# Kernel tuning notes

Measured on AMD Instinct MI355X. Metric: run time of the kernel, lower is better.

The kernel has to match this reference:

```python
import jax, jax.numpy as jnp
import numpy as np
from jax.scipy.special import logsumexp

EPS = 1e-16
SINKHORN_EPS = 0.05   # entropic regularization strength
SINKHORN_ITERS = 100  # fixed iteration count (jit-friendly)
PI = np.pi


def _p3_polarrel_from_cartesian(p):
    """(px,py,pz) [B,N,3] -> (eta_rel, phi_rel, pt_rel) [B,N,3], relative to jet."""
    px, py, pz = p[..., 0], p[..., 1], p[..., 2]
    pt = jnp.sqrt(px * px + py * py + EPS)
    phi = jnp.arctan2(py + EPS, px + EPS)
    eta = jnp.arcsinh(pz / (pt + EPS))
    # jet 3-momentum: sum over particle axis (dim -2)
    jp = p.sum(axis=-2)  # [B,3]
    jpx, jpy, jpz = jp[..., 0], jp[..., 1], jp[..., 2]
    jpt = jnp.sqrt(jpx * jpx + jpy * jpy + EPS)
    jphi = jnp.arctan2(jpy + EPS, jpx + EPS)
    jeta = jnp.arcsinh(jpz / (jpt + EPS))
    eta_rel = eta - jeta[..., None]
    phi_rel = (phi - jphi[..., None] + PI) % (2.0 * PI) - PI
    pt_rel = pt / (jpt[..., None] + EPS)
    return jnp.stack([eta_rel, phi_rel, pt_rel], axis=-1)


def _sinkhorn_emd(x, y):
    """Sinkhorn-regularized EMD between particle clouds.
    x, y: [B,N,3] of (eta_rel, phi_rel, pt_rel). Returns [B]."""
    eps = SINKHORN_EPS
    # pairwise DeltaR ground cost [B,N,N]
    deta = x[..., :, None, 0] - y[..., None, :, 0]
    dphi = x[..., :, None, 1] - y[..., None, :, 1]
    C = jnp.sqrt(deta * deta + dphi * dphi + EPS)
    # pt-based marginals (pt_rel > 0 by construction), normalized
    a = x[..., 2]
    b = y[..., 2]
    a = a / (a.sum(axis=-1, keepdims=True) + EPS)
    b = b / (b.sum(axis=-1, keepdims=True) + EPS)
    log_a = jnp.log(a + EPS)
    log_b = jnp.log(b + EPS)

    f0 = jnp.zeros_like(a)
    g0 = jnp.zeros_like(b)

    def step(carry, _):
        f, g = carry
        f = eps * (log_a - logsumexp((g[:, None, :] - C) / eps, axis=-1))
        g = eps * (log_b - logsumexp((f[:, :, None] - C) / eps, axis=-2))
        return (f, g), None

    (f, g), _ = jax.lax.scan(step, (f0, g0), None, length=SINKHORN_ITERS)
    logP = (f[:, :, None] + g[:, None, :] - C) / eps  # [B,N,N] transport plan (log)
    return jnp.sum(jnp.exp(logP) * C, axis=(-2, -1))  # [B]


def setup_inputs() -> dict:
    key = jax.random.key(0)
    k1, k2 = jax.random.split(key)
    B, N = 2048, 150
    p_recons = jax.random.normal(k1, (B, N, 3), dtype=jnp.float32)
    p_target = jax.random.normal(k2, (B, N, 3), dtype=jnp.float32)
    return {"p_recons": p_recons, "p_target": p_target}


def reference(p_recons, p_target):
    x = _p3_polarrel_from_cartesian(p_recons)
    y = _p3_polarrel_from_cartesian(p_target)
    return _sinkhorn_emd(x, y).sum(0)  # scalar, matching .sum(0) over batch
```

## Files before the change

### kernel.cpp

```cpp
#include <hip/hip_runtime.h>
#include <math.h>

#define N 150
#define NP 160
#define QUART 40
#define QUADS 10
#define BLOCK 640
#define ITERS 100
#define WARM 5

#define PI_F 3.14159265358979323846f
#define TWO_PI_F 6.28318530717958647692f
#define EPS_F 1e-16f
#define EPSLN2 0.03465735902799726f
#define INV_EPSLN2 28.853900817779268f
#define NEGBIG -1e30f

#if __has_builtin(__builtin_amdgcn_exp2f)
#define FEXP2(x) __builtin_amdgcn_exp2f(x)
#else
#define FEXP2(x) exp2f(x)
#endif
#if __has_builtin(__builtin_amdgcn_logf)
#define FLOG2(x) __builtin_amdgcn_logf(x)
#else
#define FLOG2(x) log2f(x)
#endif
#if __has_builtin(__builtin_amdgcn_rcpf)
#define FRCP(x) __builtin_amdgcn_rcpf(x)
#else
#define FRCP(x) (1.0f / (x))
#endif

typedef float f2 __attribute__((ext_vector_type(2)));
union F4P { float4 v; f2 h[2]; float f[4]; };

#if __has_builtin(__builtin_elementwise_max)
#define F2MAX(a, b) __builtin_elementwise_max((a), (b))
#else
__device__ __forceinline__ f2 f2max_fb(f2 a, f2 b) {
    f2 r; r[0] = fmaxf(a[0], b[0]); r[1] = fmaxf(a[1], b[1]); return r;
}
#define F2MAX(a, b) f2max_fb((a), (b))
#endif

#define KU(e) Ku[(e) >> 1][(e) & 1]
#define KT(e) Kt[(e) >> 1][(e) & 1]

__device__ __forceinline__ float dpp_xor1(float x) {
    return __int_as_float(__builtin_amdgcn_update_dpp(
        0, __float_as_int(x), 0xB1, 0xF, 0xF, true));
}
__device__ __forceinline__ float dpp_xor2(float x) {
    return __int_as_float(__builtin_amdgcn_update_dpp(
        0, __float_as_int(x), 0x4E, 0xF, 0xF, true));
}
__device__ __forceinline__ float quad_sum(float x) {
    x += dpp_xor1(x); x += dpp_xor2(x); return x;
}
__device__ __forceinline__ float quad_max(float x) {
    x = fmaxf(x, dpp_xor1(x)); x = fmaxf(x, dpp_xor2(x)); return x;
}

__device__ __forceinline__ float blockReduceSum(float v, float* red) {
    for (int o = 32; o > 0; o >>= 1) v += __shfl_down(v, o, 64);
    const int lane = threadIdx.x & 63;
    const int wv = threadIdx.x >> 6;
    __syncthreads();
    if (lane == 0) red[wv] = v;
    __syncthreads();
    float s = 0.f;
    #pragma unroll
    for (int i = 0; i < BLOCK / 64; ++i) s += red[i];
    return s;
}

__device__ __forceinline__ void blockReduceSum3(
    float& x, float& y, float& z, float* red)
{
    for (int o = 32; o > 0; o >>= 1) {
        x += __shfl_down(x, o, 64);
        y += __shfl_down(y, o, 64);
        z += __shfl_down(z, o, 64);
    }
    const int lane = threadIdx.x & 63;
    const int wv = threadIdx.x >> 6;
    __syncthreads();
    if (lane == 0) { red[wv] = x; red[wv + 16] = y; red[wv + 32] = z; }
    __syncthreads();
    float sx = 0.f, sy = 0.f, sz = 0.f;
    #pragma unroll
    for (int i = 0; i < BLOCK / 64; ++i) {
        sx += red[i]; sy += red[i + 16]; sz += red[i + 32];
    }
    x = sx; y = sy; z = sz;
}

__global__ __launch_bounds__(BLOCK, 2) void emd_kernel(
    const float* __restrict__ p_recons,
    const float* __restrict__ p_target,
    float* __restrict__ out)
{
    __shared__ float xeta[N], xphi[N], yeta[N], yphi[N];
    __shared__ float l2a[N], l2b[N];
    __shared__ __align__(16) float uu[NP];
    __shared__ __align__(16) float vv[NP];
    __shared__ float red[48];

    const int b = blockIdx.x;
    const int tid = threadIdx.x;

    for (int c = 0; c < 2; ++c) {
        const float* P = (c == 0 ? p_recons : p_target) + (size_t)b * (N * 3);
        float px = 0.f, py = 0.f, pz = 0.f;
        if (tid < N) {
            px = P[tid * 3 + 0];
            py = P[tid * 3 + 1];
            pz = P[tid * 3 + 2];
        }
        float jx = px, jy = py, jz = pz;
        blockReduceSum3(jx, jy, jz, red);
        const float jpt  = sqrtf(jx * jx + jy * jy + EPS_F);
        const float jphi = atan2f(jy + EPS_F, jx + EPS_F);
        const float jeta = asinhf(jz / (jpt + EPS_F));

        float ptrel = 0.f, erel = 0.f, prel = 0.f;
        if (tid < N) {
            const float pt  = sqrtf(px * px + py * py + EPS_F);
            const float phi = atan2f(py + EPS_F, px + EPS_F);
            const float eta = asinhf(pz / (pt + EPS_F));
            erel = eta - jeta;
            float d = phi - jphi + PI_F;
            d = fmodf(d, TWO_PI_F);
            if (d < 0.f) d += TWO_PI_F;
            prel = d - PI_F;
            ptrel = pt / (jpt + EPS_F);
        }
        const float spt = blockReduceSum(ptrel, red);
        if (tid < N) {
            const float aa = ptrel / (spt + EPS_F);
            if (c == 0) { xeta[tid] = erel; xphi[tid] = prel; l2a[tid] = FLOG2(aa + EPS_F); }
            else        { yeta[tid] = erel; yphi[tid] = prel; l2b[tid] = FLOG2(aa + EPS_F); }
        }
    }
    __syncthreads();

    const int r = (tid >> 2) < N ? (tid >> 2) : (N - 1);
    const int q = tid & 3;
    const bool writer = (q == 0) && ((tid >> 2) < N);
    const bool act = (tid >> 2) < N;

    f2 Ku[QUART / 2];
    f2 Kt[QUART / 2];
    {
        const float xe = xeta[r], xp = xphi[r];
        const float ye = yeta[r], yp = yphi[r];
        #pragma unroll
        for (int s = 0; s < QUART; ++s) {
            const int j = q * QUART + s;
            float ku = NEGBIG, kt = NEGBIG;
            if (j < N) {
                float de = xe - yeta[j], dp = xp - yphi[j];
                ku = -sqrtf(de * de + dp * dp + EPS_F) * INV_EPSLN2;
                de = xeta[j] - ye; dp = xphi[j] - yp;
                kt = -sqrtf(de * de + dp * dp + EPS_F) * INV_EPSLN2;
            }
            KU(s) = ku;
            KT(s) = kt;
        }
    }
    if (tid < NP) {
        const float z = (tid < N) ? 0.f : NEGBIG;
        uu[tid] = z; vv[tid] = z;
    }
    __syncthreads();

    for (int it = 0; it < WARM; ++it) {
        {
            const float4* vp = (const float4*)&vv[q * QUART];
            f2 m2 = {-3e38f, -3e38f};
            #pragma unroll
            for (int s = 0; s < QUADS; ++s) {
                F4P v4; v4.v = vp[s];
                m2 = F2MAX(m2, v4.h[0] + Ku[2*s]);
                m2 = F2MAX(m2, v4.h[1] + Ku[2*s+1]);
            }
            float mx = quad_max(fmaxf(m2[0], m2[1]));
            float s0 = 0.f, s1 = 0.f, s2 = 0.f, s3 = 0.f;
            #pragma unroll
            for (int s = 0; s < QUADS; ++s) {
                F4P v4; v4.v = vp[s];
                s0 += FEXP2(v4.f[0] + KU(4*s)   - mx);
                s1 += FEXP2(v4.f[1] + KU(4*s+1) - mx);
                s2 += FEXP2(v4.f[2] + KU(4*s+2) - mx);
                s3 += FEXP2(v4.f[3] + KU(4*s+3) - mx);
            }
            float ss = quad_sum((s0 + s1) + (s2 + s3));
            if (writer) uu[r] = l2a[r] - (mx + FLOG2(fmaxf(ss, 1e-37f)));
        }
        __syncthreads();
        {
            const float4* up = (const float4*)&uu[q * QUART];
            f2 m2 = {-3e38f, -3e38f};
            #pragma unroll
            for (int s = 0; s < QUADS; ++s) {
                F4P u4; u4.v = up[s];
                m2 = F2MAX(m2, u4.h[0] + Kt[2*s]);
                m2 = F2MAX(m2, u4.h[1] + Kt[2*s+1]);
            }
            float mx = quad_max(fmaxf(m2[0], m2[1]));
            float s0 = 0.f, s1 = 0.f, s2 = 0.f, s3 = 0.f;
            #pragma unroll
            for (int s = 0; s < QUADS; ++s) {
                F4P u4; u4.v = up[s];
                s0 += FEXP2(u4.f[0] + KT(4*s)   - mx);
                s1 += FEXP2(u4.f[1] + KT(4*s+1) - mx);
                s2 += FEXP2(u4.f[2] + KT(4*s+2) - mx);
                s3 += FEXP2(u4.f[3] + KT(4*s+3) - mx);
            }
            float ss = quad_sum((s0 + s1) + (s2 + s3));
            if (writer) vv[r] = l2b[r] - (mx + FLOG2(fmaxf(ss, 1e-37f)));
        }
        __syncthreads();
    }

    float am, bm, fin, Vh6;
    {
        const float4* vp = (const float4*)&vv[q * QUART];
        f2 m2 = {-3e38f, -3e38f};
        #pragma unroll
        for (int s = 0; s < QUADS; ++s) {
            F4P v4; v4.v = vp[s];
            m2 = F2MAX(m2, v4.h[0] + Ku[2*s]);
            m2 = F2MAX(m2, v4.h[1] + Ku[2*s+1]);
        }
        float mx = quad_max(fmaxf(m2[0], m2[1]));
        float s0 = 0.f, s1 = 0.f, s2 = 0.f, s3 = 0.f;
        #pragma unroll
        for (int s = 0; s < QUADS; ++s) {
            F4P v4; v4.v = vp[s];
            KU(4*s)   = FEXP2(v4.f[0] + KU(4*s)   - mx);
            KU(4*s+1) = FEXP2(v4.f[1] + KU(4*s+1) - mx);
            KU(4*s+2) = FEXP2(v4.f[2] + KU(4*s+2) - mx);
            KU(4*s+3) = FEXP2(v4.f[3] + KU(4*s+3) - mx);
            s0 += KU(4*s); s1 += KU(4*s+1); s2 += KU(4*s+2); s3 += KU(4*s+3);
        }
        float ss = quad_sum((s0 + s1) + (s2 + s3));
        am  = ss;
        fin = FEXP2(l2a[r]) * FRCP(ss);
        if (writer) uu[r] = l2a[r] - (mx + FLOG2(ss));
    }
    __syncthreads();
    {
        const float4* up = (const float4*)&uu[q * QUART];
        f2 m2 = {-3e38f, -3e38f};
        #pragma unroll
        for (int s = 0; s < QUADS; ++s) {
            F4P u4; u4.v = up[s];
            m2 = F2MAX(m2, u4.h[0] + Kt[2*s]);
            m2 = F2MAX(m2, u4.h[1] + Kt[2*s+1]);
        }
        float mx = quad_max(fmaxf(m2[0], m2[1]));
        float s0 = 0.f, s1 = 0.f, s2 = 0.f, s3 = 0.f;
        #pragma unroll
        for (int s = 0; s < QUADS; ++s) {
            F4P u4; u4.v = up[s];
            KT(4*s)   = FEXP2(u4.f[0] + KT(4*s)   - mx);
            KT(4*s+1) = FEXP2(u4.f[1] + KT(4*s+1) - mx);
            KT(4*s+2) = FEXP2(u4.f[2] + KT(4*s+2) - mx);
            KT(4*s+3) = FEXP2(u4.f[3] + KT(4*s+3) - mx);
            s0 += KT(4*s); s1 += KT(4*s+1); s2 += KT(4*s+2); s3 += KT(4*s+3);
        }
        float ssv = quad_sum((s0 + s1) + (s2 + s3));
        const float v5r = vv[r];
        float t = l2b[r] - (mx + FLOG2(ssv)) - v5r;
        t = fminf(t, 100.f);
        Vh6 = FEXP2(t);
        bm  = Vh6 * ssv;
    }
    __syncthreads();
    if (writer) { uu[r] = 1.0f; vv[r] = Vh6; }
    if (tid >= N && tid < NP) { uu[tid] = 0.f; vv[tid] = 0.f; }
    __syncthreads();

    for (int it = WARM + 1; it < ITERS; ++it) {
        {
            const float4* vp = (const float4*)&vv[q * QUART];
            f2 a0 = {0.f, 0.f}, a1 = {0.f, 0.f};
            #pragma unroll
            for (int s = 0; s < QUADS; ++s) {
                F4P v4; v4.v = vp[s];
                a0 += v4.h[0] * Ku[2*s];
                a1 += v4.h[1] * Ku[2*s+1];
            }
            float ss = quad_sum((a0[0] + a1[0]) + (a0[1] + a1[1]));
            if (writer) uu[r] = fminf(am * FRCP(fmaxf(ss, 1e-30f)), 1e30f);
        }
        __syncthreads();
        {
            const float4* up = (const float4*)&uu[q * QUART];
            f2 a0 = {0.f, 0.f}, a1 = {0.f, 0.f};
            #pragma unroll
            for (int s = 0; s < QUADS; ++s) {
                F4P u4; u4.v = up[s];
                a0 += u4.h[0] * Kt[2*s];
                a1 += u4.h[1] * Kt[2*s+1];
            }
            float ss = quad_sum((a0[0] + a1[0]) + (a0[1] + a1[1]));
            if (writer) vv[r] = fminf(bm * FRCP(fmaxf(ss, 1e-30f)), 1e30f);
        }
        __syncthreads();
        if (((it - WARM - 1) & 15) == 15) {
            const float4* vp = (const float4*)&vv[q * QUART];
            float M = 0.f;
            #pragma unroll
            for (int s = 0; s < QUADS; ++s) {
                F4P v4; v4.v = vp[s];
                Ku[2*s]   *= v4.h[0];
                Ku[2*s+1] *= v4.h[1];
                M = fmaxf(M, fmaxf(fmaxf(Ku[2*s][0], Ku[2*s][1]),
                                   fmaxf(Ku[2*s+1][0], Ku[2*s+1][1])));
            }
            M = quad_max(M);
            M = fmaxf(M, 1e-30f);
            const float rM = FRCP(M);
            const f2 rM2 = {rM, rM};
            #pragma unroll
            for (int i = 0; i < QUART / 2; ++i) Ku[i] *= rM2;

            const float4* up = (const float4*)&uu[q * QUART];
            float Mv = 0.f;
            #pragma unroll
            for (int s = 0; s < QUADS; ++s) {
                F4P u4; u4.v = up[s];
                Kt[2*s]   *= u4.h[0];
                Kt[2*s+1] *= u4.h[1];
                Mv = fmaxf(Mv, fmaxf(fmaxf(Kt[2*s][0], Kt[2*s][1]),
                                     fmaxf(Kt[2*s+1][0], Kt[2*s+1][1])));
            }
            Mv = quad_max(Mv);
            Mv = fmaxf(Mv, 1e-30f);
            const float rMv = FRCP(Mv);
            const f2 rMv2 = {rMv, rMv};
            #pragma unroll
            for (int i = 0; i < QUART / 2; ++i) Kt[i] *= rMv2;

            const float Uh = uu[r], Vh = vv[r];
            am  = fminf(am * rM  * FRCP(fmaxf(Uh, 1e-30f)), 1e30f);
            bm  = fminf(bm * rMv * FRCP(fmaxf(Vh, 1e-30f)), 1e30f);
            fin = fminf(fin * M * Uh, 1e30f);
            __syncthreads();
            if (writer) { uu[r] = 1.0f; vv[r] = 1.0f; }
            __syncthreads();
        }
    }

    float acc = 0.f;
    if (act) {
        const float u2 = fin * uu[r];
        const float xe = xeta[r], xp = xphi[r];
        const float4* vp = (const float4*)&vv[q * QUART];
        #pragma unroll
        for (int s = 0; s < QUADS; ++s) {
            F4P v4; v4.v = vp[s];
            #pragma unroll
            for (int k = 0; k < 4; ++k) {
                const int j = q * QUART + 4 * s + k;
                if (j < N) {
                    const float de = xe - yeta[j];
                    const float dp = xp - yphi[j];
                    const float C = sqrtf(de * de + dp * dp + EPS_F);
                    acc += u2 * v4.f[k] * KU(4 * s + k) * C;
                }
            }
        }
    }
    if (!act) acc = 0.f;
    acc = blockReduceSum(acc, red);
    if (tid == 0) atomicAdd(out, acc);
}

extern "C" void kernel_launch(void* const* d_in, const int* in_sizes, int n_in,
                              void* d_out, int out_size, void* d_ws, size_t ws_size,
                              hipStream_t stream) {
    const float* pr = (const float*)d_in[0];
    const float* pt = (const float*)d_in[1];
    float* out = (float*)d_out;
    const int B = in_sizes[0] / (N * 3);
    hipMemsetAsync(d_out, 0, sizeof(float) * out_size, stream);
    hipLaunchKernelGGL(emd_kernel, dim3(B), dim3(BLOCK), 0, stream, pr, pt, out);
}
```

Baseline: 867.9 us.

## Halve LDS reads in Sinkhorn matvec by swapping float4 chunks via DPP row rotate

Permutes each thread's column assignment so that lanes 8 apart hold swapped pairs of float4 chunks. In the main scaling loop each thread then loads only the even chunks from LDS and gets the odd chunks from its partner lane with a DPP row_ror:8, which roughly halves shared-memory read traffic per matvec. The log-domain warmup and final sum use the same permuted mapping through even/odd pointer offsets. It adds DPP moves and more complex indexing, and correctness depends on the partner lane holding the matching row's chunk.

```diff
diff --git a/kernel.cpp b/kernel.cpp
--- a/kernel.cpp
+++ b/kernel.cpp
@@ -55,6 +55,18 @@
     return __int_as_float(__builtin_amdgcn_update_dpp(
         0, __float_as_int(x), 0x4E, 0xF, 0xF, true));
 }
+__device__ __forceinline__ float dpp_ror8(float x) {
+    return __int_as_float(__builtin_amdgcn_update_dpp(
+        0, __float_as_int(x), 0x128, 0xF, 0xF, true));
+}
+__device__ __forceinline__ F4P dpp_ror8_f4(F4P x) {
+    F4P r;
+    r.f[0] = dpp_ror8(x.f[0]);
+    r.f[1] = dpp_ror8(x.f[1]);
+    r.f[2] = dpp_ror8(x.f[2]);
+    r.f[3] = dpp_ror8(x.f[3]);
+    return r;
+}
 __device__ __forceinline__ float quad_sum(float x) {
     x += dpp_xor1(x); x += dpp_xor2(x); return x;
 }
@@ -147,8 +159,11 @@
 
     const int r = (tid >> 2) < N ? (tid >> 2) : (N - 1);
     const int q = tid & 3;
+    const int hsw = (tid >> 3) & 1;
     const bool writer = (q == 0) && ((tid >> 2) < N);
     const bool act = (tid >> 2) < N;
+
+    #define COLOF(e) (((((e) >> 2) ^ hsw) << 2) + ((e) & 3))
 
     f2 Ku[QUART / 2];
     f2 Kt[QUART / 2];
@@ -157,7 +172,7 @@
         const float ye = yeta[r], yp = yphi[r];
         #pragma unroll
         for (int s = 0; s < QUART; ++s) {
-            const int j = q * QUART + s;
+            const int j = q * QUART + COLOF(s);
             float ku = NEGBIG, kt = NEGBIG;
             if (j < N) {
                 float de = xe - yeta[j], dp = xp - yphi[j];
@@ -175,13 +190,17 @@
     }
     __syncthreads();
 
+    const float4* vB = (const float4*)&vv[q * QUART];
+    const float4* uB = (const float4*)&uu[q * QUART];
+    const float4* vE = vB + hsw; const float4* vO = vB - hsw;
+    const float4* uE = uB + hsw; const float4* uO = uB - hsw;
+
     for (int it = 0; it < WARM; ++it) {
         {
-            const float4* vp = (const float4*)&vv[q * QUART];
             f2 m2 = {-3e38f, -3e38f};
             #pragma unroll
             for (int s = 0; s < QUADS; ++s) {
-                F4P v4; v4.v = vp[s];
+                F4P v4; v4.v = ((s & 1) ? vO : vE)[s];
                 m2 = F2MAX(m2, v4.h[0] + Ku[2*s]);
                 m2 = F2MAX(m2, v4.h[1] + Ku[2*s+1]);
             }
@@ -189,7 +208,7 @@
             float s0 = 0.f, s1 = 0.f, s2 = 0.f, s3 = 0.f;
             #pragma unroll
             for (int s = 0; s < QUADS; ++s) {
-                F4P v4; v4.v = vp[s];
+                F4P v4; v4.v = ((s & 1) ? vO : vE)[s];
                 s0 += FEXP2(v4.f[0] + KU(4*s)   - mx);
                 s1 += FEXP2(v4.f[1] + KU(4*s+1) - mx);
                 s2 += FEXP2(v4.f[2] + KU(4*s+2) - mx);
@@ -200,11 +219,10 @@
         }
         __syncthreads();
         {
-            const float4* up = (const float4*)&uu[q * QUART];
             f2 m2 = {-3e38f, -3e38f};
             #pragma unroll
             for (int s = 0; s < QUADS; ++s) {
-                F4P u4; u4.v = up[s];
+                F4P u4; u4.v = ((s & 1) ? uO : uE)[s];
                 m2 = F2MAX(m2, u4.h[0] + Kt[2*s]);
                 m2 = F2MAX(m2, u4.h[1] + Kt[2*s+1]);
             }
@@ -212,7 +230,7 @@
             float s0 = 0.f, s1 = 0.f, s2 = 0.f, s3 = 0.f;
             #pragma unroll
             for (int s = 0; s < QUADS; ++s) {
-                F4P u4; u4.v = up[s];
+                F4P u4; u4.v = ((s & 1) ? uO : uE)[s];
                 s0 += FEXP2(u4.f[0] + KT(4*s)   - mx);
                 s1 += FEXP2(u4.f[1] + KT(4*s+1) - mx);
                 s2 += FEXP2(u4.f[2] + KT(4*s+2) - mx);
@@ -226,11 +244,10 @@
 
     float am, bm, fin, Vh6;
     {
-        const float4* vp = (const float4*)&vv[q * QUART];
         f2 m2 = {-3e38f, -3e38f};
         #pragma unroll
         for (int s = 0; s < QUADS; ++s) {
-            F4P v4; v4.v = vp[s];
+            F4P v4; v4.v = ((s & 1) ? vO : vE)[s];
             m2 = F2MAX(m2, v4.h[0] + Ku[2*s]);
             m2 = F2MAX(m2, v4.h[1] + Ku[2*s+1]);
         }
@@ -238,7 +255,7 @@
         float s0 = 0.f, s1 = 0.f, s2 = 0.f, s3 = 0.f;
         #pragma unroll
         for (int s = 0; s < QUADS; ++s) {
-            F4P v4; v4.v = vp[s];
+            F4P v4; v4.v = ((s & 1) ? vO : vE)[s];
             KU(4*s)   = FEXP2(v4.f[0] + KU(4*s)   - mx);
             KU(4*s+1) = FEXP2(v4.f[1] + KU(4*s+1) - mx);
             KU(4*s+2) = FEXP2(v4.f[2] + KU(4*s+2) - mx);
@@ -252,11 +269,10 @@
     }
     __syncthreads();
     {
-        const float4* up = (const float4*)&uu[q * QUART];
         f2 m2 = {-3e38f, -3e38f};
         #pragma unroll
         for (int s = 0; s < QUADS; ++s) {
-            F4P u4; u4.v = up[s];
+            F4P u4; u4.v = ((s & 1) ? uO : uE)[s];
             m2 = F2MAX(m2, u4.h[0] + Kt[2*s]);
             m2 = F2MAX(m2, u4.h[1] + Kt[2*s+1]);
         }
@@ -264,7 +280,7 @@
         float s0 = 0.f, s1 = 0.f, s2 = 0.f, s3 = 0.f;
         #pragma unroll
         for (int s = 0; s < QUADS; ++s) {
-            F4P u4; u4.v = up[s];
+            F4P u4; u4.v = ((s & 1) ? uO : uE)[s];
             KT(4*s)   = FEXP2(u4.f[0] + KT(4*s)   - mx);
             KT(4*s+1) = FEXP2(u4.f[1] + KT(4*s+1) - mx);
             KT(4*s+2) = FEXP2(u4.f[2] + KT(4*s+2) - mx);
@@ -285,37 +301,40 @@
 
     for (int it = WARM + 1; it < ITERS; ++it) {
         {
-            const float4* vp = (const float4*)&vv[q * QUART];
             f2 a0 = {0.f, 0.f}, a1 = {0.f, 0.f};
             #pragma unroll
-            for (int s = 0; s < QUADS; ++s) {
-                F4P v4; v4.v = vp[s];
-                a0 += v4.h[0] * Ku[2*s];
-                a1 += v4.h[1] * Ku[2*s+1];
+            for (int k = 0; k < 5; ++k) {
+                F4P X; X.v = vE[2 * k];
+                F4P Y = dpp_ror8_f4(X);
+                a0 += X.h[0] * Ku[4*k];
+                a1 += X.h[1] * Ku[4*k+1];
+                a0 += Y.h[0] * Ku[4*k+2];
+                a1 += Y.h[1] * Ku[4*k+3];
             }
             float ss = quad_sum((a0[0] + a1[0]) + (a0[1] + a1[1]));
             if (writer) uu[r] = fminf(am * FRCP(fmaxf(ss, 1e-30f)), 1e30f);
         }
         __syncthreads();
         {
-            const float4* up = (const float4*)&uu[q * QUART];
             f2 a0 = {0.f, 0.f}, a1 = {0.f, 0.f};
             #pragma unroll
-            for (int s = 0; s < QUADS; ++s) {
-                F4P u4; u4.v = up[s];
-                a0 += u4.h[0] * Kt[2*s];
-                a1 += u4.h[1] * Kt[2*s+1];
+            for (int k = 0; k < 5; ++k) {
+                F4P X; X.v = uE[2 * k];
+                F4P Y = dpp_ror8_f4(X);
+                a0 += X.h[0] * Kt[4*k];
+                a1 += X.h[1] * Kt[4*k+1];
+                a0 += Y.h[0] * Kt[4*k+2];
+                a1 += Y.h[1] * Kt[4*k+3];
             }
             float ss = quad_sum((a0[0] + a1[0]) + (a0[1] + a1[1]));
             if (writer) vv[r] = fminf(bm * FRCP(fmaxf(ss, 1e-30f)), 1e30f);
         }
         __syncthreads();
         if (((it - WARM - 1) & 15) == 15) {
-            const float4* vp = (const float4*)&vv[q * QUART];
             float M = 0.f;
             #pragma unroll
             for (int s = 0; s < QUADS; ++s) {
-                F4P v4; v4.v = vp[s];
+                F4P v4; v4.v = ((s & 1) ? vO : vE)[s];
                 Ku[2*s]   *= v4.h[0];
                 Ku[2*s+1] *= v4.h[1];
                 M = fmaxf(M, fmaxf(fmaxf(Ku[2*s][0], Ku[2*s][1]),
@@ -328,11 +347,10 @@
             #pragma unroll
             for (int i = 0; i < QUART / 2; ++i) Ku[i] *= rM2;
 
-            const float4* up = (const float4*)&uu[q * QUART];
             float Mv = 0.f;
             #pragma unroll
             for (int s = 0; s < QUADS; ++s) {
-                F4P u4; u4.v = up[s];
+                F4P u4; u4.v = ((s & 1) ? uO : uE)[s];
                 Kt[2*s]   *= u4.h[0];
                 Kt[2*s+1] *= u4.h[1];
                 Mv = fmaxf(Mv, fmaxf(fmaxf(Kt[2*s][0], Kt[2*s][1]),
@@ -359,13 +377,12 @@
     if (act) {
         const float u2 = fin * uu[r];
         const float xe = xeta[r], xp = xphi[r];
-        const float4* vp = (const float4*)&vv[q * QUART];
         #pragma unroll
         for (int s = 0; s < QUADS; ++s) {
-            F4P v4; v4.v = vp[s];
+            F4P v4; v4.v = ((s & 1) ? vO : vE)[s];
             #pragma unroll
             for (int k = 0; k < 4; ++k) {
-                const int j = q * QUART + 4 * s + k;
+                const int j = q * QUART + COLOF(4 * s + k);
                 if (j < N) {
                     const float de = xe - yeta[j];
                     const float dp = xp - yphi[j];
```

Result: slower. 1.049 ms (+20.8%).
